# Kernel optimization log

Measured on AMD Instinct MI355X. Metric: run time of the kernel, lower is better.

Reference implementation:

```python
import jax, jax.numpy as jnp
import numpy as np

OUT = 7            # output_size
SR = 2             # sampling_ratio
SCALES = (0.25, 0.125, 0.0625, 0.03125)  # P2..P5
CANON_S = 224.0
CANON_L = 4.0
LVL_EPS = 1e-6
K_MIN, K_MAX = 2, 5  # -log2(scales[0]), -log2(scales[-1])


def setup_inputs() -> dict:
    key = jax.random.key(0)
    ks = jax.random.split(key, 6)
    B, C, N = 2, 256, 256
    sizes = (200, 100, 50, 25)
    inp = {}
    for i, (k, hw) in enumerate(zip(ks[:4], sizes)):
        inp[f"feat{i}"] = jax.random.normal(k, (B, C, hw, hw), dtype=jnp.float32)
    x1y1 = jax.random.uniform(ks[4], (B, N, 2), minval=0.0, maxval=600.0)
    wh = jax.random.uniform(ks[5], (B, N, 2), minval=16.0, maxval=256.0)
    boxes = jnp.concatenate([x1y1, jnp.minimum(x1y1 + wh, 800.0)], axis=-1)
    inp["boxes"] = boxes.astype(jnp.float32)
    return inp


def _roi_align(feat, rois, scale):
    """torchvision RoIAlign (aligned=False). feat [B,C,H,W], rois [N,5] (bidx,x1,y1,x2,y2)."""
    B, C, H, W = feat.shape
    bidx = rois[:, 0].astype(jnp.int32)
    x1 = rois[:, 1] * scale
    y1 = rois[:, 2] * scale
    x2 = rois[:, 3] * scale
    y2 = rois[:, 4] * scale
    roi_w = jnp.maximum(x2 - x1, 1.0)
    roi_h = jnp.maximum(y2 - y1, 1.0)
    bin_h = roi_h / OUT
    bin_w = roi_w / OUT
    g = jnp.arange(OUT * SR)
    bin_idx = (g // SR).astype(feat.dtype)
    sub = (g % SR).astype(feat.dtype) + 0.5
    # sample coordinates [N, G] with G = OUT*SR
    ys = y1[:, None] + bin_idx * bin_h[:, None] + sub * bin_h[:, None] / SR
    xs = x1[:, None] + bin_idx * bin_w[:, None] + sub * bin_w[:, None] / SR
    vy = (ys >= -1.0) & (ys <= H)
    vx = (xs >= -1.0) & (xs <= W)
    y = jnp.clip(ys, 0.0, H - 1.0)
    x = jnp.clip(xs, 0.0, W - 1.0)
    y0 = jnp.floor(y).astype(jnp.int32)
    x0 = jnp.floor(x).astype(jnp.int32)
    y1i = jnp.minimum(y0 + 1, H - 1)
    x1i = jnp.minimum(x0 + 1, W - 1)
    ly = y - y0
    lx = x - x0
    hy = 1.0 - ly
    hx = 1.0 - lx

    def gather(yi, xi):
        # advanced indices at dims 0,2,3 with slice at dim 1 -> [N, G, G, C]
        return feat[bidx[:, None, None], :, yi[:, :, None], xi[:, None, :]]

    v = (gather(y0, x0) * (hy[:, :, None] * hx[:, None, :])[..., None]
         + gather(y0, x1i) * (hy[:, :, None] * lx[:, None, :])[..., None]
         + gather(y1i, x0) * (ly[:, :, None] * hx[:, None, :])[..., None]
         + gather(y1i, x1i) * (ly[:, :, None] * lx[:, None, :])[..., None])
    mask = (vy[:, :, None] & vx[:, None, :])[..., None]
    v = jnp.where(mask, v, 0.0)                       # [N, G, G, C]
    n = v.shape[0]
    v = v.reshape(n, OUT, SR, OUT, SR, C).mean(axis=(2, 4))  # avg pool per bin
    return jnp.transpose(v, (0, 3, 1, 2))             # [N, C, OUT, OUT]


def reference(feat0, feat1, feat2, feat3, boxes):
    feats = [feat0, feat1, feat2, feat3]
    B, N = boxes.shape[:2]
    flat = boxes.reshape(B * N, 4)
    ids = jnp.repeat(jnp.arange(B, dtype=flat.dtype), N)[:, None]
    rois = jnp.concatenate([ids, flat], axis=1)       # [B*N, 5]
    # FPN level assignment heuristic (LevelMapper)
    area = (flat[:, 2] - flat[:, 0]) * (flat[:, 3] - flat[:, 1])
    s = jnp.sqrt(area)
    lvl = jnp.floor(CANON_L + jnp.log2(s / CANON_S) + LVL_EPS)
    levels = jnp.clip(lvl, K_MIN, K_MAX).astype(jnp.int32) - K_MIN
    # Pool every roi at every level (static shapes), then select by level,
    # equivalent math to the gather/scatter-merge in the original.
    pooled = jnp.stack([_roi_align(f, rois, sc) for f, sc in zip(feats, SCALES)], axis=0)
    return pooled[levels, jnp.arange(B * N)]          # [B*N, C, OUT, OUT]
```

## Files before the change

### kernel.cpp

```cpp
#include <hip/hip_runtime.h>
#include <hip/hip_fp16.h>


#define ROI_OUT 7
#define NSAMP   14
#define C_TOT   256
#define N_PER_B 256
#define BINS    49
#define TOT_HW  53125

#define NTILE_X 832

__device__ __forceinline__ int swz4(int c) { return ((c ^ (c >> 3)) & 7) << 2; }

__global__ __launch_bounds__(256)
void repack_kernel(const float* __restrict__ f0, const float* __restrict__ f1,
                   const float* __restrict__ f2, const float* __restrict__ f3,
                   __half* __restrict__ ws)
{
    __shared__ float tile[64 * 64];

    const int tx = blockIdx.x;
    const float* feat; int HW, base, hw0;
    if (tx < 625)      { feat = f0; HW = 40000; base = 0;     hw0 = tx * 64; }
    else if (tx < 782) { feat = f1; HW = 10000; base = 40000; hw0 = (tx - 625) * 64; }
    else if (tx < 822) { feat = f2; HW = 2500;  base = 50000; hw0 = (tx - 782) * 64; }
    else               { feat = f3; HW = 625;   base = 52500; hw0 = (tx - 822) * 64; }

    const int c0 = blockIdx.y * 64;
    const int b  = blockIdx.z;
    const float* src = feat + ((size_t)(b * C_TOT + c0)) * (size_t)HW + hw0;

    const int t    = threadIdx.x;
    const int hwq  = (t & 15) * 4;
    const int crow = t >> 4;

    const bool fast = (hw0 + 64 <= HW) && ((HW & 3) == 0);

    if (fast) {
        #pragma unroll
        for (int i = 0; i < 4; ++i) {
            int c = crow + 16 * i;
            float4 v = *(const float4*)(src + (size_t)c * HW + hwq);
            *(float4*)&tile[c * 64 + (hwq ^ swz4(c))] = v;
        }
    } else {
        #pragma unroll
        for (int i = 0; i < 4; ++i) {
            int c = crow + 16 * i;
            float* drow = &tile[c * 64 + (hwq ^ swz4(c))];
            #pragma unroll
            for (int k = 0; k < 4; ++k) {
                int hw = hw0 + hwq + k;
                drow[k] = (hw < HW) ? src[(size_t)c * HW + hwq + k] : 0.0f;
            }
        }
    }
    __syncthreads();

    const int cc0 = (t & 7) * 8;
    __half* dst = ws + ((size_t)b * TOT_HW + base) * C_TOT + c0 + cc0;
    #pragma unroll
    for (int it = 0; it < 2; ++it) {
        int hwr = (t >> 3) + 32 * it;
        int hw  = hw0 + hwr;
        if (hw < HW) {
            int hb = hwr & ~3, ho = hwr & 3;
            __half2 h[4];
            #pragma unroll
            for (int j = 0; j < 8; j += 2) {
                int ca = cc0 + j, cb = cc0 + j + 1;
                float fa = tile[ca * 64 + ((hb ^ swz4(ca)) + ho)];
                float fb = tile[cb * 64 + ((hb ^ swz4(cb)) + ho)];
                h[j >> 1] = __floats2half2_rn(fa, fb);
            }
            *(float4*)(dst + (size_t)hw * C_TOT) = *(const float4*)h;
        }
    }
}

__global__ __launch_bounds__(256)
void msroi_main(const __half* __restrict__ ws, const float* __restrict__ boxes,
                float* __restrict__ out)
{
    __shared__ float oacc[C_TOT * BINS];
    __shared__ int4  pY[NSAMP], pX[NSAMP];

    const int tid = threadIdx.x;
    const int roi = blockIdx.x;
    const int b   = roi >> 8;

    const float* bxp = boxes + (size_t)roi * 4;
    float bx1 = bxp[0], by1 = bxp[1], bx2 = bxp[2], by2 = bxp[3];
    float area = (bx2 - bx1) * (by2 - by1);
    float s    = sqrtf(area);
    float lvlf = floorf(4.0f + log2f(s * (1.0f / 224.0f)) + 1e-6f);
    lvlf = fminf(fmaxf(lvlf, 2.0f), 5.0f);
    int level = (int)lvlf - 2;

    int H, W, lvbase; float scale;
    switch (level) {
        case 0:  H = 200; W = 200; lvbase = 0;     scale = 0.25f;    break;
        case 1:  H = 100; W = 100; lvbase = 40000; scale = 0.125f;   break;
        case 2:  H = 50;  W = 50;  lvbase = 50000; scale = 0.0625f;  break;
        default: H = 25;  W = 25;  lvbase = 52500; scale = 0.03125f; break;
    }

    float x1 = bx1 * scale, y1 = by1 * scale;
    float roi_w = fmaxf(bx2 * scale - x1, 1.0f);
    float roi_h = fmaxf(by2 * scale - y1, 1.0f);
    float bin_w = roi_w * (1.0f / ROI_OUT);
    float bin_h = roi_h * (1.0f / ROI_OUT);

    if (tid < 2 * NSAMP) {
        bool isy = tid >= NSAMP;
        int  j   = isy ? tid - NSAMP : tid;
        int  pb  = j >> 1, sub = j & 1;
        float start = isy ? y1 : x1;
        float bsz   = isy ? bin_h : bin_w;
        int   lim   = isy ? H : W;
        float ss = start + (float)pb * bsz + ((float)sub + 0.5f) * bsz * 0.5f;
        float v  = (ss >= -1.0f && ss <= (float)lim) ? 1.0f : 0.0f;
        float cc = fminf(fmaxf(ss, 0.0f), (float)lim - 1.0f);
        int   i0 = (int)floorf(cc);
        int   i1 = min(i0 + 1, lim - 1);
        float l  = cc - (float)i0;
        int4 pk; pk.x = i0; pk.y = i1;
        pk.z = __float_as_int(l); pk.w = __float_as_int(v);
        if (isy) pY[j] = pk; else pX[j] = pk;
    }
    __syncthreads();

    const int wave = tid >> 6;
    const int lane = tid & 63;
    const int c    = lane * 4;
    const __half* base = ws + ((size_t)b * TOT_HW + lvbase) * C_TOT + c;

    for (int bin = wave; bin < BINS; bin += 4) {
        int ph = bin / ROI_OUT;
        int pw = bin - ph * ROI_OUT;
        float a0 = 0.f, a1 = 0.f, a2 = 0.f, a3 = 0.f;

        #pragma unroll
        for (int sy = 0; sy < 2; ++sy) {
            int4 py  = pY[2 * ph + sy];
            float ly = __int_as_float(py.z);
            float vy = __int_as_float(py.w);
            float hy = 1.0f - ly;
            #pragma unroll
            for (int sx = 0; sx < 2; ++sx) {
                int4 px  = pX[2 * pw + sx];
                float lx = __int_as_float(px.z);
                float vv = vy * __int_as_float(px.w);
                float hx = 1.0f - lx;
                float w00 = vv * hy * hx, w01 = vv * hy * lx;
                float w10 = vv * ly * hx, w11 = vv * ly * lx;

                const __half2* p00 = (const __half2*)(base + (size_t)(py.x * W + px.x) * C_TOT);
                const __half2* p01 = (const __half2*)(base + (size_t)(py.x * W + px.y) * C_TOT);
                const __half2* p10 = (const __half2*)(base + (size_t)(py.y * W + px.x) * C_TOT);
                const __half2* p11 = (const __half2*)(base + (size_t)(py.y * W + px.y) * C_TOT);

                float2 g0, g1;
                g0 = __half22float2(p00[0]); g1 = __half22float2(p00[1]);
                a0 += w00 * g0.x; a1 += w00 * g0.y; a2 += w00 * g1.x; a3 += w00 * g1.y;
                g0 = __half22float2(p01[0]); g1 = __half22float2(p01[1]);
                a0 += w01 * g0.x; a1 += w01 * g0.y; a2 += w01 * g1.x; a3 += w01 * g1.y;
                g0 = __half22float2(p10[0]); g1 = __half22float2(p10[1]);
                a0 += w10 * g0.x; a1 += w10 * g0.y; a2 += w10 * g1.x; a3 += w10 * g1.y;
                g0 = __half22float2(p11[0]); g1 = __half22float2(p11[1]);
                a0 += w11 * g0.x; a1 += w11 * g0.y; a2 += w11 * g1.x; a3 += w11 * g1.y;
            }
        }
        oacc[(c + 0) * BINS + bin] = a0 * 0.25f;
        oacc[(c + 1) * BINS + bin] = a1 * 0.25f;
        oacc[(c + 2) * BINS + bin] = a2 * 0.25f;
        oacc[(c + 3) * BINS + bin] = a3 * 0.25f;
    }
    __syncthreads();

    float4*       o4 = (float4*)(out + (size_t)roi * (C_TOT * BINS));
    const float4* s4 = (const float4*)oacc;
    for (int j = tid; j < (C_TOT * BINS) / 4; j += 256) o4[j] = s4[j];
}

__global__ __launch_bounds__(256)
void msroi_direct(const float* __restrict__ f0, const float* __restrict__ f1,
                  const float* __restrict__ f2, const float* __restrict__ f3,
                  const float* __restrict__ boxes, float* __restrict__ out, int total)
{
    int e = blockIdx.x * 256 + threadIdx.x;
    if (e >= total) return;
    int bin = e % BINS;
    int c   = (e / BINS) % C_TOT;
    int roi = e / (BINS * C_TOT);
    int b   = roi / N_PER_B;

    const float* bx = boxes + (size_t)roi * 4;
    float bx1 = bx[0], by1 = bx[1], bx2 = bx[2], by2 = bx[3];
    float area = (bx2 - bx1) * (by2 - by1);
    float s    = sqrtf(area);
    float lvlf = floorf(4.0f + log2f(s * (1.0f / 224.0f)) + 1e-6f);
    lvlf = fminf(fmaxf(lvlf, 2.0f), 5.0f);
    int level = (int)lvlf - 2;

    const float* feat; int H, W; float scale;
    switch (level) {
        case 0:  feat = f0; H = 200; W = 200; scale = 0.25f;    break;
        case 1:  feat = f1; H = 100; W = 100; scale = 0.125f;   break;
        case 2:  feat = f2; H = 50;  W = 50;  scale = 0.0625f;  break;
        default: feat = f3; H = 25;  W = 25;  scale = 0.03125f; break;
    }
    float x1 = bx1 * scale, y1 = by1 * scale;
    float roi_w = fmaxf(bx2 * scale - x1, 1.0f);
    float roi_h = fmaxf(by2 * scale - y1, 1.0f);
    float bin_w = roi_w * (1.0f / ROI_OUT);
    float bin_h = roi_h * (1.0f / ROI_OUT);
    int ph = bin / ROI_OUT, pw = bin - ph * ROI_OUT;
    const float* plane = feat + ((size_t)(b * C_TOT + c)) * (size_t)(H * W);
    float Hf = (float)H, Wf = (float)W, acc = 0.0f;
    #pragma unroll
    for (int sy = 0; sy < 2; ++sy) {
        float ys = y1 + (float)ph * bin_h + ((float)sy + 0.5f) * bin_h * 0.5f;
        float vy = (ys >= -1.0f && ys <= Hf) ? 1.0f : 0.0f;
        float y  = fminf(fmaxf(ys, 0.0f), Hf - 1.0f);
        int   y0 = (int)floorf(y);
        int   y1i = min(y0 + 1, H - 1);
        float ly = y - (float)y0, hy = 1.0f - ly;
        int ro0 = y0 * W, ro1 = y1i * W;
        #pragma unroll
        for (int sx = 0; sx < 2; ++sx) {
            float xs = x1 + (float)pw * bin_w + ((float)sx + 0.5f) * bin_w * 0.5f;
            float vx = (xs >= -1.0f && xs <= Wf) ? 1.0f : 0.0f;
            float x  = fminf(fmaxf(xs, 0.0f), Wf - 1.0f);
            int   x0 = (int)floorf(x);
            int   x1i = min(x0 + 1, W - 1);
            float lx = x - (float)x0, hx = 1.0f - lx;
            float v00 = plane[ro0 + x0],  v01 = plane[ro0 + x1i];
            float v10 = plane[ro1 + x0],  v11 = plane[ro1 + x1i];
            acc += vy * vx * (hy * (hx * v00 + lx * v01) + ly * (hx * v10 + lx * v11));
        }
    }
    out[e] = acc * 0.25f;
}

extern "C" void kernel_launch(void* const* d_in, const int* in_sizes, int n_in,
                              void* d_out, int out_size, void* d_ws, size_t ws_size,
                              hipStream_t stream)
{
    const float* f0    = (const float*)d_in[0];
    const float* f1    = (const float*)d_in[1];
    const float* f2    = (const float*)d_in[2];
    const float* f3    = (const float*)d_in[3];
    const float* boxes = (const float*)d_in[4];
    float* out = (float*)d_out;

    const size_t ws_needed = (size_t)2 * TOT_HW * C_TOT * sizeof(__half);
    if (ws_size >= ws_needed) {
        __half* ws = (__half*)d_ws;
        hipLaunchKernelGGL(repack_kernel, dim3(NTILE_X, 4, 2), dim3(256), 0, stream,
                           f0, f1, f2, f3, ws);
        hipLaunchKernelGGL(msroi_main, dim3(2 * N_PER_B), dim3(256), 0, stream,
                           ws, boxes, out);
    } else {
        int total = out_size;
        hipLaunchKernelGGL(msroi_direct, dim3((total + 255) / 256), dim3(256), 0, stream,
                           f0, f1, f2, f3, boxes, out, total);
    }
}
```

Baseline: 51.12 us.

## Repack features into 64-channel planes with larger 256-pixel tiles

The repack kernel now processes 256 spatial positions per block instead of 64 and converts to half precision before storing to shared memory. It writes the workspace as four separate 64-channel planes per level rather than one interleaved 256-channel layout. The gather kernel's addressing is changed to match, so each quarter of a wave reads its own plane. The aim is fewer repack blocks with more loads in flight, and better locality for the bilinear gathers. The cost is more registers per thread and different coalescing of gather loads.

```diff
diff --git a/kernel.cpp b/kernel.cpp
--- a/kernel.cpp
+++ b/kernel.cpp
@@ -9,72 +9,80 @@
 #define BINS    49
 #define TOT_HW  53125
 
-#define NTILE_X 832
-
-__device__ __forceinline__ int swz4(int c) { return ((c ^ (c >> 3)) & 7) << 2; }
+#define NTILE_X 210
+
+__device__ __forceinline__ int swz(int c) { return (c ^ (c >> 3)) & 7; }
 
 __global__ __launch_bounds__(256)
 void repack_kernel(const float* __restrict__ f0, const float* __restrict__ f1,
                    const float* __restrict__ f2, const float* __restrict__ f3,
                    __half* __restrict__ ws)
 {
-    __shared__ float tile[64 * 64];
+    __shared__ __half tile[64 * 256];
 
     const int tx = blockIdx.x;
     const float* feat; int HW, base, hw0;
-    if (tx < 625)      { feat = f0; HW = 40000; base = 0;     hw0 = tx * 64; }
-    else if (tx < 782) { feat = f1; HW = 10000; base = 40000; hw0 = (tx - 625) * 64; }
-    else if (tx < 822) { feat = f2; HW = 2500;  base = 50000; hw0 = (tx - 782) * 64; }
-    else               { feat = f3; HW = 625;   base = 52500; hw0 = (tx - 822) * 64; }
-
-    const int c0 = blockIdx.y * 64;
+    if (tx < 157)      { feat = f0; HW = 40000; base = 0;     hw0 = tx * 256; }
+    else if (tx < 197) { feat = f1; HW = 10000; base = 40000; hw0 = (tx - 157) * 256; }
+    else if (tx < 207) { feat = f2; HW = 2500;  base = 50000; hw0 = (tx - 197) * 256; }
+    else               { feat = f3; HW = 625;   base = 52500; hw0 = (tx - 207) * 256; }
+
+    const int g  = blockIdx.y;
+    const int c0 = g * 64;
     const int b  = blockIdx.z;
-    const float* src = feat + ((size_t)(b * C_TOT + c0)) * (size_t)HW + hw0;
-
-    const int t    = threadIdx.x;
-    const int hwq  = (t & 15) * 4;
-    const int crow = t >> 4;
-
-    const bool fast = (hw0 + 64 <= HW) && ((HW & 3) == 0);
+    const float* src = feat + ((size_t)(b * C_TOT + c0)) * (size_t)HW;
+
+    const int t   = threadIdx.x;
+    const int lc  = t >> 6;
+    const int hwb = (t & 63) * 4;
+
+    const bool fast = (hw0 + 256 <= HW) && ((HW & 3) == 0);
 
     if (fast) {
-        #pragma unroll
-        for (int i = 0; i < 4; ++i) {
-            int c = crow + 16 * i;
-            float4 v = *(const float4*)(src + (size_t)c * HW + hwq);
-            *(float4*)&tile[c * 64 + (hwq ^ swz4(c))] = v;
+        float4 v[16];
+        #pragma unroll
+        for (int i = 0; i < 16; ++i) {
+            int c = lc + 4 * i;
+            v[i] = *(const float4*)(src + (size_t)c * HW + hw0 + hwb);
+        }
+        #pragma unroll
+        for (int i = 0; i < 16; ++i) {
+            int c   = lc + 4 * i;
+            int idx = c * 256 + (hwb ^ (swz(c) << 2));
+            *(__half2*)(tile + idx)     = __floats2half2_rn(v[i].x, v[i].y);
+            *(__half2*)(tile + idx + 2) = __floats2half2_rn(v[i].z, v[i].w);
         }
     } else {
         #pragma unroll
-        for (int i = 0; i < 4; ++i) {
-            int c = crow + 16 * i;
-            float* drow = &tile[c * 64 + (hwq ^ swz4(c))];
+        for (int i = 0; i < 16; ++i) {
+            int c = lc + 4 * i;
+            float f[4];
             #pragma unroll
             for (int k = 0; k < 4; ++k) {
-                int hw = hw0 + hwq + k;
-                drow[k] = (hw < HW) ? src[(size_t)c * HW + hwq + k] : 0.0f;
+                int hw = hw0 + hwb + k;
+                f[k] = (hw < HW) ? src[(size_t)c * HW + hw] : 0.0f;
             }
+            int idx = c * 256 + (hwb ^ (swz(c) << 2));
+            *(__half2*)(tile + idx)     = __floats2half2_rn(f[0], f[1]);
+            *(__half2*)(tile + idx + 2) = __floats2half2_rn(f[2], f[3]);
         }
     }
     __syncthreads();
 
-    const int cc0 = (t & 7) * 8;
-    __half* dst = ws + ((size_t)b * TOT_HW + base) * C_TOT + c0 + cc0;
+    const int coct = (t & 7) * 8;
+    __half* plane = ws + ((size_t)b * TOT_HW + base) * C_TOT + (size_t)g * (size_t)HW * 64;
     #pragma unroll
-    for (int it = 0; it < 2; ++it) {
+    for (int it = 0; it < 8; ++it) {
         int hwr = (t >> 3) + 32 * it;
         int hw  = hw0 + hwr;
         if (hw < HW) {
-            int hb = hwr & ~3, ho = hwr & 3;
-            __half2 h[4];
+            __half h[8];
             #pragma unroll
-            for (int j = 0; j < 8; j += 2) {
-                int ca = cc0 + j, cb = cc0 + j + 1;
-                float fa = tile[ca * 64 + ((hb ^ swz4(ca)) + ho)];
-                float fb = tile[cb * 64 + ((hb ^ swz4(cb)) + ho)];
-                h[j >> 1] = __floats2half2_rn(fa, fb);
+            for (int j = 0; j < 8; ++j) {
+                int c = coct + j;
+                h[j] = tile[c * 256 + (hwr ^ (swz(c) << 2))];
             }
-            *(float4*)(dst + (size_t)hw * C_TOT) = *(const float4*)h;
+            *(float4*)(plane + (size_t)hw * 64 + coct) = *(const float4*)h;
         }
     }
 }
@@ -134,7 +142,9 @@
     const int wave = tid >> 6;
     const int lane = tid & 63;
     const int c    = lane * 4;
-    const __half* base = ws + ((size_t)b * TOT_HW + lvbase) * C_TOT + c;
+    const __half* gbase = ws + ((size_t)b * TOT_HW + lvbase) * C_TOT
+                             + (size_t)(lane >> 4) * (size_t)(H * W) * 64
+                             + (lane & 15) * 4;
 
     for (int bin = wave; bin < BINS; bin += 4) {
         int ph = bin / ROI_OUT;
@@ -156,10 +166,10 @@
                 float w00 = vv * hy * hx, w01 = vv * hy * lx;
                 float w10 = vv * ly * hx, w11 = vv * ly * lx;
 
-                const __half2* p00 = (const __half2*)(base + (size_t)(py.x * W + px.x) * C_TOT);
-                const __half2* p01 = (const __half2*)(base + (size_t)(py.x * W + px.y) * C_TOT);
-                const __half2* p10 = (const __half2*)(base + (size_t)(py.y * W + px.x) * C_TOT);
-                const __half2* p11 = (const __half2*)(base + (size_t)(py.y * W + px.y) * C_TOT);
+                const __half2* p00 = (const __half2*)(gbase + (size_t)(py.x * W + px.x) * 64);
+                const __half2* p01 = (const __half2*)(gbase + (size_t)(py.x * W + px.y) * 64);
+                const __half2* p10 = (const __half2*)(gbase + (size_t)(py.y * W + px.x) * 64);
+                const __half2* p11 = (const __half2*)(gbase + (size_t)(py.y * W + px.y) * 64);
 
                 float2 g0, g1;
                 g0 = __half22float2(p00[0]); g1 = __half22float2(p00[1]);
```

Result: slower. 55.68 us (+8.9%).

## Split repacked features into 64-channel planes and load tiles via global_load_lds

Applied to the files above, without the earlier changes.

The repack kernel now copies global memory straight into LDS with the global_load_lds builtin, applying the swizzle on the source address, in place of register-staged float4 loads. The workspace layout changes from pixel-major with 256 channels to four channel-group planes of 64 channels each, and the main kernel's gather addressing is updated to match. Each bilinear corner fetch now touches four 128-byte segments spread across separate planes rather than one contiguous 512-byte row, which could hurt gather locality. The repack write side also shrinks to 8-byte stores.

```diff
diff --git a/kernel.cpp b/kernel.cpp
--- a/kernel.cpp
+++ b/kernel.cpp
@@ -11,7 +11,10 @@
 
 #define NTILE_X 832
 
-__device__ __forceinline__ int swz4(int c) { return ((c ^ (c >> 3)) & 7) << 2; }
+#define SWZG(c) ((((c) ^ ((c) >> 3)) & 7) << 2)
+
+typedef const __attribute__((address_space(1))) float* gas1_t;
+typedef __attribute__((address_space(3))) float*       las3_t;
 
 __global__ __launch_bounds__(256)
 void repack_kernel(const float* __restrict__ f0, const float* __restrict__ f1,
@@ -27,54 +30,61 @@
     else if (tx < 822) { feat = f2; HW = 2500;  base = 50000; hw0 = (tx - 782) * 64; }
     else               { feat = f3; HW = 625;   base = 52500; hw0 = (tx - 822) * 64; }
 
-    const int c0 = blockIdx.y * 64;
+    const int g  = blockIdx.y;
+    const int c0 = g * 64;
     const int b  = blockIdx.z;
     const float* src = feat + ((size_t)(b * C_TOT + c0)) * (size_t)HW + hw0;
 
-    const int t    = threadIdx.x;
-    const int hwq  = (t & 15) * 4;
-    const int crow = t >> 4;
+    const int t = threadIdx.x;
+    const int w = t >> 6;
+    const int l = t & 63;
 
     const bool fast = (hw0 + 64 <= HW) && ((HW & 3) == 0);
 
     if (fast) {
+        const int cq = l >> 4;
+        const int hl = (l & 15) * 4;
         #pragma unroll
         for (int i = 0; i < 4; ++i) {
-            int c = crow + 16 * i;
-            float4 v = *(const float4*)(src + (size_t)c * HW + hwq);
-            *(float4*)&tile[c * 64 + (hwq ^ swz4(c))] = v;
+            int q = 4 * w + i;
+            int c = 4 * q + cq;
+            const float* gp = src + (size_t)c * HW + (hl ^ SWZG(c));
+            __builtin_amdgcn_global_load_lds((gas1_t)(const void*)gp,
+                                             (las3_t)(void*)(tile + q * 256),
+                                             16, 0, 0);
         }
     } else {
+        const int hl = (t & 15) * 4;
+        const int cr = t >> 4;
         #pragma unroll
         for (int i = 0; i < 4; ++i) {
-            int c = crow + 16 * i;
-            float* drow = &tile[c * 64 + (hwq ^ swz4(c))];
+            int c  = cr + 16 * i;
+            int ps = hl ^ SWZG(c);
             #pragma unroll
-            for (int k = 0; k < 4; ++k) {
-                int hw = hw0 + hwq + k;
-                drow[k] = (hw < HW) ? src[(size_t)c * HW + hwq + k] : 0.0f;
+            for (int j = 0; j < 4; ++j) {
+                int srchw = ps + j;
+                float v = (srchw < HW - hw0) ? src[(size_t)c * HW + srchw] : 0.0f;
+                tile[c * 64 + hl + j] = v;
             }
         }
     }
     __syncthreads();
 
-    const int cc0 = (t & 7) * 8;
-    __half* dst = ws + ((size_t)b * TOT_HW + base) * C_TOT + c0 + cc0;
+    __half* plane = ws + ((size_t)b * TOT_HW + base) * C_TOT
+                       + (size_t)g * (size_t)HW * 64 + (size_t)hw0 * 64;
+    const int c4 = (l & 15) * 4;
     #pragma unroll
-    for (int it = 0; it < 2; ++it) {
-        int hwr = (t >> 3) + 32 * it;
-        int hw  = hw0 + hwr;
-        if (hw < HW) {
-            int hb = hwr & ~3, ho = hwr & 3;
-            __half2 h[4];
-            #pragma unroll
-            for (int j = 0; j < 8; j += 2) {
-                int ca = cc0 + j, cb = cc0 + j + 1;
-                float fa = tile[ca * 64 + ((hb ^ swz4(ca)) + ho)];
-                float fb = tile[cb * 64 + ((hb ^ swz4(cb)) + ho)];
-                h[j >> 1] = __floats2half2_rn(fa, fb);
-            }
-            *(float4*)(dst + (size_t)hw * C_TOT) = *(const float4*)h;
+    for (int i = 0; i < 4; ++i) {
+        int hw = 16 * w + 4 * i + (l >> 4);
+        if (hw0 + hw < HW) {
+            float v0 = tile[(c4 + 0) * 64 + (hw ^ SWZG(c4 + 0))];
+            float v1 = tile[(c4 + 1) * 64 + (hw ^ SWZG(c4 + 1))];
+            float v2 = tile[(c4 + 2) * 64 + (hw ^ SWZG(c4 + 2))];
+            float v3 = tile[(c4 + 3) * 64 + (hw ^ SWZG(c4 + 3))];
+            __half2 hh[2];
+            hh[0] = __floats2half2_rn(v0, v1);
+            hh[1] = __floats2half2_rn(v2, v3);
+            *(float2*)(plane + (size_t)hw * 64 + c4) = *(const float2*)hh;
         }
     }
 }
@@ -134,7 +144,9 @@
     const int wave = tid >> 6;
     const int lane = tid & 63;
     const int c    = lane * 4;
-    const __half* base = ws + ((size_t)b * TOT_HW + lvbase) * C_TOT + c;
+    const __half* gbase = ws + ((size_t)b * TOT_HW + lvbase) * C_TOT
+                             + (size_t)(lane >> 4) * (size_t)(H * W) * 64
+                             + (lane & 15) * 4;
 
     for (int bin = wave; bin < BINS; bin += 4) {
         int ph = bin / ROI_OUT;
@@ -156,10 +168,10 @@
                 float w00 = vv * hy * hx, w01 = vv * hy * lx;
                 float w10 = vv * ly * hx, w11 = vv * ly * lx;
 
-                const __half2* p00 = (const __half2*)(base + (size_t)(py.x * W + px.x) * C_TOT);
-                const __half2* p01 = (const __half2*)(base + (size_t)(py.x * W + px.y) * C_TOT);
-                const __half2* p10 = (const __half2*)(base + (size_t)(py.y * W + px.x) * C_TOT);
-                const __half2* p11 = (const __half2*)(base + (size_t)(py.y * W + px.y) * C_TOT);
+                const __half2* p00 = (const __half2*)(gbase + (size_t)(py.x * W + px.x) * 64);
+                const __half2* p01 = (const __half2*)(gbase + (size_t)(py.x * W + px.y) * 64);
+                const __half2* p10 = (const __half2*)(gbase + (size_t)(py.y * W + px.x) * 64);
+                const __half2* p11 = (const __half2*)(gbase + (size_t)(py.y * W + px.y) * 64);
 
                 float2 g0, g1;
                 g0 = __half22float2(p00[0]); g1 = __half22float2(p00[1]);
```

Result: no change. 50.95 us (-0.3%).
